# Optimization experiments

Measured on AMD Instinct MI355X. Metric: run time of the kernel, lower is better.

Reference implementation:

```python
import jax, jax.numpy as jnp
import numpy as np

DIM = 8          # per-head dim
EPS = 1e-15
GROUPS_PW = 192  # 3 * heads = 3 * 64


def _conv(x, w, groups=1, pad=0):
    return jax.lax.conv_general_dilated(
        x, w, window_strides=(1, 1), padding=[(pad, pad), (pad, pad)],
        dimension_numbers=('NCHW', 'OIHW', 'NCHW'), feature_group_count=groups)


def setup_inputs() -> dict:
    key = jax.random.key(0)
    k0, k1, k2, k3, k4 = jax.random.split(key, 5)
    B, C, H, W = 4, 512, 64, 64
    td = 512  # heads * dim
    x = jax.random.normal(k0, (B, C, H, W), jnp.float32)
    w_qkv = jax.random.normal(k1, (3 * td, C, 1, 1), jnp.float32) * 0.05
    w_dw = jax.random.normal(k2, (3 * td, 1, 5, 5), jnp.float32) * 0.05
    w_pw = jax.random.normal(k3, (3 * td, (3 * td) // GROUPS_PW, 1, 1), jnp.float32) * 0.05
    w_proj = jax.random.normal(k4, (C, 2 * td, 1, 1), jnp.float32) * 0.05
    return {'x': x, 'w_qkv': w_qkv, 'w_dw': w_dw, 'w_pw': w_pw, 'w_proj': w_proj}


def reference(x, w_qkv, w_dw, w_pw, w_proj):
    # qkv projection (1x1 conv, no bias, no norm/act per config)
    qkv = _conv(x, w_qkv)  # [B, 3*td, H, W]
    # multi-scale aggregation: depthwise 5x5 then grouped 1x1 (groups = 3*heads)
    agg = _conv(_conv(qkv, w_dw, groups=w_dw.shape[0], pad=2), w_pw, groups=GROUPS_PW)
    qkv = jnp.concatenate([qkv, agg], axis=1)  # [B, 6*td, H, W]

    B, _, H, W = qkv.shape
    qkv = qkv.reshape(B, -1, 3 * DIM, H * W)  # [B, h_eff, 3*dim, HW]
    q = jax.nn.relu(qkv[:, :, :DIM])          # [B, h, dim, HW]
    k = jax.nn.relu(qkv[:, :, DIM:2 * DIM])   # [B, h, dim, HW]
    v = qkv[:, :, 2 * DIM:]                   # [B, h, dim, HW]
    # pad v with a row of ones -> normalization trick
    v = jnp.pad(v, ((0, 0), (0, 0), (0, 1), (0, 0)), constant_values=1.0)
    # linear attention via associativity: (v k^T) q
    vk = jnp.einsum('bhdn,bhen->bhde', v, k)   # [B, h, dim+1, dim]
    out = jnp.einsum('bhde,bhen->bhdn', vk, q) # [B, h, dim+1, HW]
    out = out[:, :, :-1] / (out[:, :, -1:] + EPS)
    out = out.reshape(B, -1, H, W)             # [B, 2*td, H, W]
    return x + _conv(out, w_proj)
```

## Files before the change

kernel.cpp:

```cpp
#include <hip/hip_runtime.h>
#include <hip/hip_bf16.h>
#include <cstdint>
#include <cstddef>


typedef __hip_bfloat16 bf16;
typedef __attribute__((ext_vector_type(8))) short short8;
typedef __attribute__((ext_vector_type(4))) float f32x4;

__device__ __forceinline__ float b2f(bf16 v) { return __bfloat162float(v); }
__device__ __forceinline__ bf16 f2b(float v) { return __float2bfloat16(v); }
__device__ __forceinline__ float us2f(unsigned short u) {
    return __uint_as_float(((unsigned)u) << 16);
}

__device__ __forceinline__ float dot2bf(unsigned p, unsigned wp, float acc) {
#if __has_builtin(__builtin_amdgcn_fdot2_f32_bf16)
    typedef __attribute__((ext_vector_type(2))) __bf16 bf16x2;
    return __builtin_amdgcn_fdot2_f32_bf16(
        __builtin_bit_cast(bf16x2, p), __builtin_bit_cast(bf16x2, wp),
        acc, false);
#else
    return acc
        + us2f((unsigned short)(p & 0xffffu))  * us2f((unsigned short)(wp & 0xffffu))
        + us2f((unsigned short)(p >> 16))      * us2f((unsigned short)(wp >> 16));
#endif
}

__device__ __forceinline__ void async16(void* lds_base, const void* gaddr) {
    __builtin_amdgcn_global_load_lds(
        (const __attribute__((address_space(1))) unsigned int*)gaddr,
        (__attribute__((address_space(3))) unsigned int*)lds_base,
        16, 0, 0);
}

__global__ __launch_bounds__(256) void convert_kernel(
    const float* __restrict__ src, bf16* __restrict__ dst, int n)
{
    int i = blockIdx.x * 256 + threadIdx.x;
    if (i < n) dst[i] = f2b(src[i]);
}

__global__ __launch_bounds__(256) void transpose_x_kernel(
    const float* __restrict__ x, bf16* __restrict__ x_t)
{
    __shared__ bf16 tile[32][33];
    const int b = blockIdx.z;
    const int c0 = blockIdx.y * 32;
    const int n0 = blockIdx.x * 32;
    const int tx = threadIdx.x & 31, ty = threadIdx.x >> 5;
    #pragma unroll
    for (int i = 0; i < 32; i += 8)
        tile[ty + i][tx] = f2b(x[((size_t)b * 512 + c0 + ty + i) * 4096 + n0 + tx]);
    __syncthreads();
    #pragma unroll
    for (int i = 0; i < 32; i += 8)
        x_t[((size_t)b * 4096 + n0 + ty + i) * 512 + c0 + tx] = tile[tx][ty + i];
}

template <bool PROJ>
__global__ __launch_bounds__(256) void mfma_gemm_kernel(
    const bf16* __restrict__ A, const bf16* __restrict__ xt_or_qkv,
    const bf16* __restrict__ agg, const float* __restrict__ X,
    void* __restrict__ Cout, int M, int K)
{
    constexpr int N = 4096;
    const int b = blockIdx.z;
    const int m_blk = blockIdx.y * 128;
    const int n_blk = blockIdx.x * 128;

    __shared__ short As[128 * 32];
    __shared__ short Bs[128 * 32];

    const int tid = threadIdx.x;
    const int lane = tid & 63, wave = tid >> 6;
    const int wm = (wave >> 1) * 64, wn = (wave & 1) * 64;
    const int fm = lane & 15, fq = lane >> 4;

    f32x4 acc[4][4] = {};

    const short* Ag = (const short*)A;
    const short* Btg = PROJ ? nullptr
        : (const short*)(xt_or_qkv + (size_t)b * N * 512);

    for (int k0 = 0; k0 < K; k0 += 32) {
        #pragma unroll
        for (int t0 = 0; t0 < 2; ++t0) {
            int t = wave + t0 * 4;
            int row = m_blk + t * 16 + (lane >> 2);
            int col = k0 + (lane & 3) * 8;
            async16(&As[t * 512], Ag + (size_t)row * K + col);
        }
        #pragma unroll
        for (int t0 = 0; t0 < 2; ++t0) {
            int t = wave + t0 * 4;
            int n = n_blk + t * 16 + (lane >> 2);
            if (!PROJ) {
                int col = k0 + (lane & 3) * 8;
                async16(&Bs[t * 512], Btg + (size_t)n * 512 + col);
            } else {
                int h = (k0 >> 3) + (lane & 3);
                const bf16* chunk = (h < 64 ? xt_or_qkv : agg) +
                    ((size_t)b * 1536 + (size_t)(h & 63) * 24 + 16) * 4096;
                async16(&Bs[t * 512], chunk + (size_t)n * 8);
            }
        }
        __syncthreads();

        short8 af[4], bfv[4];
        #pragma unroll
        for (int i = 0; i < 4; ++i)
            af[i] = *(const short8*)&As[(wm + i * 16 + fm) * 32 + fq * 8];
        #pragma unroll
        for (int j = 0; j < 4; ++j)
            bfv[j] = *(const short8*)&Bs[(wn + j * 16 + fm) * 32 + fq * 8];
        #pragma unroll
        for (int i = 0; i < 4; ++i)
            #pragma unroll
            for (int j = 0; j < 4; ++j)
                acc[i][j] = __builtin_amdgcn_mfma_f32_16x16x32_bf16(
                    af[i], bfv[j], acc[i][j], 0, 0, 0);
        __syncthreads();
    }

    if (!PROJ) {
        bf16* Cb = (bf16*)Cout + (size_t)b * M * N;
        #pragma unroll
        for (int i = 0; i < 4; ++i)
            #pragma unroll
            for (int j = 0; j < 4; ++j) {
                int n = n_blk + wn + j * 16 + fm;
                #pragma unroll
                for (int r = 0; r < 4; ++r) {
                    int m = m_blk + wm + i * 16 + fq * 4 + r;
                    Cb[(size_t)m * N + n] = f2b(acc[i][j][r]);
                }
            }
    } else {
        float* Ob = (float*)Cout + (size_t)b * M * N;
        const float* Xb = X + (size_t)b * M * N;
        #pragma unroll
        for (int i = 0; i < 4; ++i)
            #pragma unroll
            for (int j = 0; j < 4; ++j) {
                int n = n_blk + wn + j * 16 + fm;
                #pragma unroll
                for (int r = 0; r < 4; ++r) {
                    int m = m_blk + wm + i * 16 + fq * 4 + r;
                    size_t off = (size_t)m * N + n;
                    Ob[off] = acc[i][j][r] + Xb[off];
                }
            }
    }
}

__global__ __launch_bounds__(256) void dwpw_kernel(
    const bf16* __restrict__ qkv, const float* __restrict__ w_dw,
    const float* __restrict__ w_pw, bf16* __restrict__ agg)
{
    const int bg = blockIdx.y;
    const int b = bg / 192;
    const int g = bg - b * 192;
    const int y0 = blockIdx.x * 32;

    __shared__ unsigned s_wdwp[8][16];
    __shared__ float s_wpw[8][8];

    const int tid = threadIdx.x;

    if (tid < 120) {
        int c = tid / 15, s = tid - c * 15;
        int i = s / 3, p = s - i * 3;
        int idx = i * 5 + p * 2;
        float w0 = w_dw[(size_t)(g * 8 + c) * 25 + idx];
        float w1 = (p < 2) ? w_dw[(size_t)(g * 8 + c) * 25 + idx + 1] : 0.f;
        unsigned u0 = __builtin_bit_cast(unsigned short, f2b(w0));
        unsigned u1 = __builtin_bit_cast(unsigned short, f2b(w1));
        s_wdwp[c][s] = u0 | (u1 << 16);
    }
    if (tid < 64)
        s_wpw[tid >> 3][tid & 7] = w_pw[(size_t)(g * 8 + (tid >> 3)) * 8 + (tid & 7)];
    __syncthreads();

    const int py = tid >> 3;
    const int sx = tid & 7;
    const int yq = y0 + py;
    const size_t chan_base = ((size_t)b * 1536 + g * 8) * 4096;

    const unsigned lo_keep = (sx > 0) ? 0xFFFFFFFFu : 0u;
    const unsigned hi_keep = (sx < 7) ? 0xFFFFFFFFu : 0u;

    float dwv[8][8];
    #pragma unroll
    for (int c = 0; c < 8; ++c) {
        unsigned wpq[16];
        #pragma unroll
        for (int q = 0; q < 4; ++q)
            *(uint4*)&wpq[q * 4] = *(const uint4*)&s_wdwp[c][q * 4];

        const char* cbase = (const char*)(qkv + chan_base + (size_t)c * 4096);
        float a[8] = {};
        #pragma unroll
        for (int i = 0; i < 5; ++i) {
            const int y = yq + i - 2;
            const bool row_ok = ((unsigned)y < 64u);
            const int yc = row_ok ? y : 0;
            const char* rowp = cbase + yc * 128;
            uint4 mid = *(const uint4*)(rowp + 16 * sx);
            const unsigned m = row_ok ? 0xFFFFFFFFu : 0u;

            unsigned lo = (unsigned)__shfl_up((int)mid.w, 1, 64);
            unsigned hi = (unsigned)__shfl_down((int)mid.x, 1, 64);

            unsigned W0 = lo & m & lo_keep;
            unsigned W1 = mid.x & m, W2 = mid.y & m;
            unsigned W3 = mid.z & m, W4 = mid.w & m;
            unsigned W5 = hi & m & hi_keep;
            unsigned S0 = __builtin_amdgcn_alignbit(W1, W0, 16);
            unsigned S1 = __builtin_amdgcn_alignbit(W2, W1, 16);
            unsigned S2 = __builtin_amdgcn_alignbit(W3, W2, 16);
            unsigned S3 = __builtin_amdgcn_alignbit(W4, W3, 16);
            unsigned S4 = __builtin_amdgcn_alignbit(W5, W4, 16);
            unsigned S5 = W5 >> 16;

            unsigned w01 = wpq[i * 3], w23 = wpq[i * 3 + 1], w4z = wpq[i * 3 + 2];
            a[0] = dot2bf(W0, w01, dot2bf(W1, w23, dot2bf(W2, w4z, a[0])));
            a[2] = dot2bf(W1, w01, dot2bf(W2, w23, dot2bf(W3, w4z, a[2])));
            a[4] = dot2bf(W2, w01, dot2bf(W3, w23, dot2bf(W4, w4z, a[4])));
            a[6] = dot2bf(W3, w01, dot2bf(W4, w23, dot2bf(W5, w4z, a[6])));
            a[1] = dot2bf(S0, w01, dot2bf(S1, w23, dot2bf(S2, w4z, a[1])));
            a[3] = dot2bf(S1, w01, dot2bf(S2, w23, dot2bf(S3, w4z, a[3])));
            a[5] = dot2bf(S2, w01, dot2bf(S3, w23, dot2bf(S4, w4z, a[5])));
            a[7] = dot2bf(S3, w01, dot2bf(S4, w23, dot2bf(S5, w4z, a[7])));
        }
        #pragma unroll
        for (int x = 0; x < 8; ++x) dwv[c][x] = a[x];
    }

    const size_t out_pix = (size_t)yq * 64 + 8 * sx;
    #pragma unroll
    for (int o = 0; o < 8; ++o) {
        float wv[8];
        *(float4*)&wv[0] = *(const float4*)&s_wpw[o][0];
        *(float4*)&wv[4] = *(const float4*)&s_wpw[o][4];
        float s[8] = {};
        #pragma unroll
        for (int i = 0; i < 8; ++i)
            #pragma unroll
            for (int x = 0; x < 8; ++x) s[x] += dwv[i][x] * wv[i];
        union { bf16 hv[8]; uint4 u; } pk;
        #pragma unroll
        for (int x = 0; x < 8; ++x) pk.hv[x] = f2b(s[x]);
        *(uint4*)(agg + chan_base + (size_t)o * 4096 + out_pix) = pk.u;
    }
}

__global__ __launch_bounds__(512) void vk_kernel(
    const bf16* __restrict__ qkv, const bf16* __restrict__ agg,
    float* __restrict__ vk)
{
    const int bh = blockIdx.x;
    const int b = bh >> 7;
    const int h = bh & 127;
    const bf16* base = (h < 64)
        ? (qkv + ((size_t)b * 1536 + h * 24) * 4096)
        : (agg + ((size_t)b * 1536 + (h - 64) * 24) * 4096);

    const int tid = threadIdx.x;
    const int n0 = tid * 8;

    short8 kr[8], vr[8];
    #pragma unroll
    for (int e = 0; e < 8; ++e)
        kr[e] = *(const short8*)&base[(size_t)(8 + e) * 4096 + n0];
    #pragma unroll
    for (int d = 0; d < 8; ++d)
        vr[d] = *(const short8*)&base[(size_t)(16 + d) * 4096 + n0];

    float acc[9][8] = {};
    #pragma unroll
    for (int t = 0; t < 8; ++t) {
        float kt[8], vt[8];
        #pragma unroll
        for (int e = 0; e < 8; ++e)
            kt[e] = fmaxf(us2f((unsigned short)kr[e][t]), 0.f);
        #pragma unroll
        for (int d = 0; d < 8; ++d)
            vt[d] = us2f((unsigned short)vr[d][t]);
        #pragma unroll
        for (int d = 0; d < 8; ++d)
            #pragma unroll
            for (int e = 0; e < 8; ++e)
                acc[d][e] += vt[d] * kt[e];
        #pragma unroll
        for (int e = 0; e < 8; ++e) acc[8][e] += kt[e];
    }

    __shared__ float red[8][72];
    const int lane = tid & 63, wave = tid >> 6;
    #pragma unroll
    for (int d = 0; d < 9; ++d) {
        #pragma unroll
        for (int e = 0; e < 8; ++e) {
            float v = acc[d][e];
            #pragma unroll
            for (int off = 32; off > 0; off >>= 1) v += __shfl_down(v, off, 64);
            if (lane == 0) red[wave][d * 8 + e] = v;
        }
    }
    __syncthreads();
    if (tid < 72) {
        float v = 0.f;
        #pragma unroll
        for (int w = 0; w < 8; ++w) v += red[w][tid];
        vk[(size_t)bh * 72 + tid] = v;
    }
}

__global__ __launch_bounds__(256) void attn_out_kernel(
    bf16* __restrict__ qkv, bf16* __restrict__ agg,
    const float* __restrict__ vk)
{
    const int b = blockIdx.z;
    const int h = blockIdx.y;
    const int n0 = (blockIdx.x * 256 + threadIdx.x) * 8;
    bf16* base = (h < 64)
        ? (qkv + ((size_t)b * 1536 + h * 24) * 4096)
        : (agg + ((size_t)b * 1536 + (h - 64) * 24) * 4096);

    __shared__ float s_vk[72];
    if (threadIdx.x < 72)
        s_vk[threadIdx.x] = vk[((size_t)b * 128 + h) * 72 + threadIdx.x];
    __syncthreads();

    short8 qr[8];
    #pragma unroll
    for (int e = 0; e < 8; ++e)
        qr[e] = *(const short8*)&base[(size_t)e * 4096 + n0];

    char* outp = (char*)(base + (size_t)16 * 4096) + (size_t)n0 * 16;
    #pragma unroll
    for (int t = 0; t < 8; ++t) {
        float q[8];
        #pragma unroll
        for (int e = 0; e < 8; ++e)
            q[e] = fmaxf(us2f((unsigned short)qr[e][t]), 0.f);

        float o[9];
        #pragma unroll
        for (int d = 0; d < 9; ++d) {
            float s = 0.f;
            #pragma unroll
            for (int e = 0; e < 8; ++e) s += s_vk[d * 8 + e] * q[e];
            o[d] = s;
        }
        const float denom = o[8] + 1e-15f;

        union { bf16 hv[8]; uint4 u; } pk;
        #pragma unroll
        for (int d = 0; d < 8; ++d) pk.hv[d] = f2b(o[d] / denom);
        *(uint4*)(outp + (size_t)t * 16) = pk.u;
    }
}

extern "C" void kernel_launch(void* const* d_in, const int* in_sizes, int n_in,
                              void* d_out, int out_size, void* d_ws, size_t ws_size,
                              hipStream_t stream) {
    const float* x      = (const float*)d_in[0];
    const float* w_qkv  = (const float*)d_in[1];
    const float* w_dw   = (const float*)d_in[2];
    const float* w_pw   = (const float*)d_in[3];
    const float* w_proj = (const float*)d_in[4];

    char* ws = (char*)d_ws;
    bf16* w_qkv_bf  = (bf16*)ws;
    bf16* w_proj_bf = (bf16*)(ws + 1572864);
    float* vkbf     = (float*)(ws + 1572864 + 1048576);
    bf16* x_t       = (bf16*)(ws + 1572864 + 1048576 + 147456);
    bf16* qkv       = x_t + (size_t)4 * 4096 * 512;
    bf16* agg       = qkv + (size_t)4 * 1536 * 4096;

    convert_kernel<<<3072, 256, 0, stream>>>(w_qkv, w_qkv_bf, 786432);
    convert_kernel<<<2048, 256, 0, stream>>>(w_proj, w_proj_bf, 524288);
    transpose_x_kernel<<<dim3(128, 16, 4), 256, 0, stream>>>(x, x_t);

    mfma_gemm_kernel<false><<<dim3(32, 12, 4), 256, 0, stream>>>(
        w_qkv_bf, x_t, nullptr, nullptr, qkv, 1536, 512);

    dwpw_kernel<<<dim3(2, 768), 256, 0, stream>>>(qkv, w_dw, w_pw, agg);

    vk_kernel<<<dim3(512), 512, 0, stream>>>(qkv, agg, vkbf);

    attn_out_kernel<<<dim3(2, 128, 4), 256, 0, stream>>>(qkv, agg, vkbf);

    mfma_gemm_kernel<true><<<dim3(32, 4, 4), 256, 0, stream>>>(
        w_proj_bf, qkv, agg, x, d_out, 512, 1024);
}
```

Baseline: 256.8 us.

## Load MFMA GEMM fragments directly from global memory, dropping LDS staging

```diff
diff --git a/kernel.cpp b/kernel.cpp
--- a/kernel.cpp
+++ b/kernel.cpp
@@ -27,13 +27,6 @@
 #endif
 }
 
-__device__ __forceinline__ void async16(void* lds_base, const void* gaddr) {
-    __builtin_amdgcn_global_load_lds(
-        (const __attribute__((address_space(1))) unsigned int*)gaddr,
-        (__attribute__((address_space(3))) unsigned int*)lds_base,
-        16, 0, 0);
-}
-
 __global__ __launch_bounds__(256) void convert_kernel(
     const float* __restrict__ src, bf16* __restrict__ dst, int n)
 {
@@ -69,9 +62,6 @@
     const int m_blk = blockIdx.y * 128;
     const int n_blk = blockIdx.x * 128;
 
-    __shared__ short As[128 * 32];
-    __shared__ short Bs[128 * 32];
-
     const int tid = threadIdx.x;
     const int lane = tid & 63, wave = tid >> 6;
     const int wm = (wave >> 1) * 64, wn = (wave & 1) * 64;
@@ -79,48 +69,51 @@
 
     f32x4 acc[4][4] = {};
 
-    const short* Ag = (const short*)A;
-    const short* Btg = PROJ ? nullptr
-        : (const short*)(xt_or_qkv + (size_t)b * N * 512);
+    const short* ap[4];
+    #pragma unroll
+    for (int i = 0; i < 4; ++i)
+        ap[i] = (const short*)A + (size_t)(m_blk + wm + i * 16 + fm) * K + fq * 8;
+
+    const short* bp[4];
+    unsigned n8[4];
+    if (!PROJ) {
+        const short* Btg = (const short*)(xt_or_qkv + (size_t)b * N * 512);
+        #pragma unroll
+        for (int j = 0; j < 4; ++j)
+            bp[j] = Btg + (size_t)(n_blk + wn + j * 16 + fm) * 512 + fq * 8;
+    } else {
+        #pragma unroll
+        for (int j = 0; j < 4; ++j)
+            n8[j] = (unsigned)(n_blk + wn + j * 16 + fm) * 8;
+    }
 
     for (int k0 = 0; k0 < K; k0 += 32) {
-        #pragma unroll
-        for (int t0 = 0; t0 < 2; ++t0) {
-            int t = wave + t0 * 4;
-            int row = m_blk + t * 16 + (lane >> 2);
-            int col = k0 + (lane & 3) * 8;
-            async16(&As[t * 512], Ag + (size_t)row * K + col);
-        }
-        #pragma unroll
-        for (int t0 = 0; t0 < 2; ++t0) {
-            int t = wave + t0 * 4;
-            int n = n_blk + t * 16 + (lane >> 2);
-            if (!PROJ) {
-                int col = k0 + (lane & 3) * 8;
-                async16(&Bs[t * 512], Btg + (size_t)n * 512 + col);
-            } else {
-                int h = (k0 >> 3) + (lane & 3);
-                const bf16* chunk = (h < 64 ? xt_or_qkv : agg) +
-                    ((size_t)b * 1536 + (size_t)(h & 63) * 24 + 16) * 4096;
-                async16(&Bs[t * 512], chunk + (size_t)n * 8);
+        short8 af[4], bfv[4];
+        #pragma unroll
+        for (int i = 0; i < 4; ++i) {
+            af[i] = *(const short8*)ap[i];
+            ap[i] += 32;
+        }
+        if (!PROJ) {
+            #pragma unroll
+            for (int j = 0; j < 4; ++j) {
+                bfv[j] = *(const short8*)bp[j];
+                bp[j] += 32;
             }
-        }
-        __syncthreads();
-
-        short8 af[4], bfv[4];
-        #pragma unroll
-        for (int i = 0; i < 4; ++i)
-            af[i] = *(const short8*)&As[(wm + i * 16 + fm) * 32 + fq * 8];
-        #pragma unroll
-        for (int j = 0; j < 4; ++j)
-            bfv[j] = *(const short8*)&Bs[(wn + j * 16 + fm) * 32 + fq * 8];
+        } else {
+            const int h = (k0 >> 3) + fq;
+            const short* cb = (const short*)((h < 64 ? xt_or_qkv : agg) +
+                ((size_t)b * 1536 + (size_t)(h & 63) * 24 + 16) * 4096);
+            #pragma unroll
+            for (int j = 0; j < 4; ++j)
+                bfv[j] = *(const short8*)(cb + n8[j]);
+        }
         #pragma unroll
         for (int i = 0; i < 4; ++i)
             #pragma unroll
             for (int j = 0; j < 4; ++j)
                 acc[i][j] = __builtin_amdgcn_mfma_f32_16x16x32_bf16(
                     af[i], bfv[j], acc[i][j], 0, 0, 0);
-        __syncthreads();
     }
 
     if (!PROJ) {
```

Measured after the change: 314.0 us. +22.3%, slower.
